# Kernel optimization log

Measured on AMD Instinct MI355X. Metric: run time of the kernel, lower is better.

Reference implementation:

```python
import jax, jax.numpy as jnp
import numpy as np
import math

B, T, C = 4, 2048, 1024
H = 16
D = C // H  # head dim = 64


def setup_inputs() -> dict:
    key = jax.random.key(0)
    k1, k2, k3 = jax.random.split(key, 3)
    x = jax.random.normal(k1, (B, T, C), dtype=jnp.float32)
    # torch nn.Linear weight layout: [out_features, in_features]
    w_attn = jax.random.normal(k2, (3 * C, C), dtype=jnp.float32) * (1.0 / math.sqrt(C))
    w_proj = jax.random.normal(k3, (C, C), dtype=jnp.float32) * (1.0 / math.sqrt(C))
    return {"x": x, "w_attn": w_attn, "w_proj": w_proj}


def reference(x, w_attn, w_proj):
    b, t, c = x.shape
    # qkv projection: Linear(C, 3C) with no bias -> x @ w_attn.T
    qkv = jnp.einsum('btc,oc->bto', x, w_attn)  # [B,T,3C]
    q, k, v = jnp.split(qkv, 3, axis=-1)
    # [B,T,C] -> [B,H,T,D]
    q = q.reshape(b, t, H, D).transpose(0, 2, 1, 3)
    k = k.reshape(b, t, H, D).transpose(0, 2, 1, 3)
    v = v.reshape(b, t, H, D).transpose(0, 2, 1, 3)
    scale = 1.0 / math.sqrt(D)
    att = jnp.einsum('bhqd,bhkd->bhqk', q, k) * scale  # [B,H,T,T]
    # NOTE: faithful to source — the naive branch applies NO causal mask
    att = jax.nn.softmax(att, axis=-1)
    y = jnp.einsum('bhqk,bhkd->bhqd', att, v)  # [B,H,T,D]
    y = y.transpose(0, 2, 1, 3).reshape(b, t, c)
    return jnp.einsum('btc,oc->bto', y, w_proj)
```

## Files before the change

### kernel.cpp

```cpp
#include <hip/hip_runtime.h>

#define T_SEQ 2048
#define C_DIM 1024
#define H_NUM 16
#define H_D   64
#define B_NUM 4
#define M_ROWS 8192

typedef __attribute__((ext_vector_type(4))) float f32x4;
typedef __attribute__((ext_vector_type(8))) short bf16x8;

__device__ __forceinline__ unsigned short f2bf(float f) {
  union { float f; unsigned int u; } a;
  a.f = f;
  unsigned int u = a.u;
  u += 0x7fffu + ((u >> 16) & 1u);
  return (unsigned short)(u >> 16);
}

__device__ __forceinline__ unsigned int fbits(float f) {
  union { float f; unsigned int u; } a; a.f = f; return a.u;
}

__device__ __forceinline__ unsigned int pack_hi(float a, float b) {
#if __has_builtin(__builtin_amdgcn_perm)
  return __builtin_amdgcn_perm(fbits(b), fbits(a), 0x07060302u);
#else
  return (fbits(b) & 0xffff0000u) | (fbits(a) >> 16);
#endif
}

__device__ __forceinline__ void gload_lds16(const unsigned short* g, unsigned short* l) {
  __builtin_amdgcn_global_load_lds(
      (const __attribute__((address_space(1))) unsigned int*)g,
      (__attribute__((address_space(3))) unsigned int*)l, 16, 0, 0);
}

__global__ __launch_bounds__(256) void cast_all_kernel(const float* __restrict__ x,
                                                       const float* __restrict__ wa,
                                                       const float* __restrict__ wp,
                                                       unsigned short* __restrict__ xb,
                                                       unsigned short* __restrict__ wab,
                                                       unsigned short* __restrict__ wpb) {
  int i = blockIdx.x * 256 + threadIdx.x;
  const float* src;
  unsigned short* dst;
  int off;
  if (i < 2097152) {
    src = x; dst = xb; off = i;
  } else if (i < 2883584) {
    src = wa; dst = wab; off = i - 2097152;
  } else {
    src = wp; dst = wpb; off = i - 2883584;
  }
  float4 v = reinterpret_cast<const float4*>(src)[off];
  ushort4 o;
  o.x = f2bf(v.x); o.y = f2bf(v.y); o.z = f2bf(v.z); o.w = f2bf(v.w);
  reinterpret_cast<ushort4*>(dst)[off] = o;
}

template <int EPI>
__global__ __launch_bounds__(256, 4) void gemm_bt_kernel(
    const unsigned short* __restrict__ A,
    const unsigned short* __restrict__ Bw,
    unsigned short* __restrict__ q_ws,
    unsigned short* __restrict__ k_ws,
    unsigned short* __restrict__ v_ws,
    float* __restrict__ outf) {
  constexpr int NN = (EPI == 0) ? 3072 : 1024;
  constexpr int KK = 1024;
  constexpr int NBC = NN / 128;
  constexpr int KT = KK / 64;

  __shared__ unsigned short lds[16384];

  const int bid = blockIdx.x;
  const int rb = bid / NBC, cb = bid % NBC;
  const int t = threadIdx.x;
  const int w = t >> 6, l = t & 63;
  const int wr = w >> 1, wc = w & 1;
  const int lq = l & 15, lg = l >> 4;

  const size_t a_base = (size_t)(rb * 128) * KK;
  const size_t b_base = (size_t)(cb * 128) * KK;

  int s_row[4], s_gs[4];
#pragma unroll
  for (int i = 0; i < 4; ++i) {
    int c = t + 256 * i;
    s_row[i] = c >> 3;
    s_gs[i] = (c & 7) ^ (s_row[i] & 7);
  }

  f32x4 acc[4][4] = {};

  for (int kt = 0; kt < KT; ++kt) {
    const int ko = kt * 64;
#pragma unroll
    for (int i = 0; i < 4; ++i) {
      unsigned short* la = &lds[(t + 256 * i) * 8];
      gload_lds16(A + a_base + (size_t)s_row[i] * KK + ko + s_gs[i] * 8, la);
      gload_lds16(Bw + b_base + (size_t)s_row[i] * KK + ko + s_gs[i] * 8, la + 8192);
    }
    __syncthreads();

#pragma unroll
    for (int kk = 0; kk < 2; ++kk) {
      const int sg = kk * 4 + lg;
      bf16x8 af[4], bfv[4];
#pragma unroll
      for (int i = 0; i < 4; ++i) {
        int R = wr * 64 + i * 16 + lq;
        af[i] = *reinterpret_cast<const bf16x8*>(&lds[(R * 8 + (sg ^ (R & 7))) * 8]);
      }
#pragma unroll
      for (int j = 0; j < 4; ++j) {
        int R = wc * 64 + j * 16 + lq;
        bfv[j] = *reinterpret_cast<const bf16x8*>(&lds[8192 + (R * 8 + (sg ^ (R & 7))) * 8]);
      }
#pragma unroll
      for (int i = 0; i < 4; ++i)
#pragma unroll
        for (int j = 0; j < 4; ++j)
          acc[i][j] = __builtin_amdgcn_mfma_f32_16x16x32_bf16(af[i], bfv[j], acc[i][j], 0, 0, 0);
    }
    __syncthreads();
  }

#pragma unroll
  for (int i = 0; i < 4; ++i) {
#pragma unroll
    for (int j = 0; j < 4; ++j) {
#pragma unroll
      for (int r = 0; r < 4; ++r) {
        int m = rb * 128 + wr * 64 + i * 16 + lg * 4 + r;
        int n = cb * 128 + wc * 64 + j * 16 + lq;
        float v = acc[i][j][r];
        if (EPI == 0) {
          int which = n >> 10;
          int h = (n >> 6) & 15;
          int d = n & 63;
          int b = m >> 11;
          int tt = m & 2047;
          int bh = b * H_NUM + h;
          if (which == 0) {
            q_ws[((size_t)bh * T_SEQ + tt) * H_D + d] = f2bf(v * 0.18033688f);
          } else if (which == 1) {
            k_ws[((size_t)bh * T_SEQ + tt) * H_D + d] = f2bf(v);
          } else {
            int k0 = tt & 63;
            int tp = (tt & ~63) | ((k0 & 12) << 1) | ((k0 & 48) >> 3) | (k0 & 1) | ((k0 & 2) << 4);
            v_ws[((size_t)bh * H_D + d) * T_SEQ + tp] = f2bf(v);
          }
        } else {
          outf[(size_t)m * 1024 + n] = v;
        }
      }
    }
  }
}

__global__ __launch_bounds__(256, 2) void attn_kernel(
    const unsigned short* __restrict__ qw,
    const unsigned short* __restrict__ kw,
    const unsigned short* __restrict__ vtw,
    unsigned short* __restrict__ yw) {
  __shared__ unsigned short kv_lds[3][8192];

  const int bid = blockIdx.x;
  const int bh = (bid & 7) * 8 + ((bid >> 3) & 7);
  const int qblk = bid >> 6;

  const int t = threadIdx.x;
  const int w = t >> 6, l = t & 63;
  const int lq = l & 15, lg = l >> 4;
  const int qbase = qblk * 256 + w * 64;
  const size_t head_off = (size_t)bh * T_SEQ * H_D;

  bf16x8 aq[4][2];
#pragma unroll
  for (int qg = 0; qg < 4; ++qg)
#pragma unroll
    for (int kk = 0; kk < 2; ++kk)
      aq[qg][kk] = *reinterpret_cast<const bf16x8*>(
          qw + head_off + (size_t)(qbase + qg * 16 + lq) * H_D + kk * 32 + lg * 8);

  const unsigned short* sbase[4];
  int sstep[4];
#pragma unroll
  for (int i = 0; i < 4; ++i) {
    int c = w * 64 + l + 256 * i;
    if (c < 512) {
      int row = c >> 3, sl = (c & 7) ^ (row & 7);
      sbase[i] = kw + head_off + row * H_D + sl * 8;
      sstep[i] = 64 * H_D;
    } else {
      int c2 = c - 512;
      int row = c2 >> 3, sl = (c2 & 7) ^ (row & 7);
      sbase[i] = vtw + head_off + (size_t)row * T_SEQ + sl * 8;
      sstep[i] = 64;
    }
  }

  unsigned short* bA = &kv_lds[0][0];
  unsigned short* bB = &kv_lds[1][0];
  unsigned short* bC = &kv_lds[2][0];

#define STAGE(KV, DST)                                                              \
  { _Pragma("unroll")                                                               \
    for (int i = 0; i < 4; ++i)                                                     \
      gload_lds16(sbase[i] + (size_t)(KV) * sstep[i], (DST) + (w * 64 + 256 * i) * 8); }

  STAGE(0, bA)
  STAGE(1, bB)

  f32x4 y[4][4] = {};
  float lrow[4] = {0.f, 0.f, 0.f, 0.f};
  union pa_t { bf16x8 v; unsigned int u[4]; };

  for (int kv = 0; kv < T_SEQ / 64; ++kv) {
    if (kv == T_SEQ / 64 - 1) {
      asm volatile("s_waitcnt vmcnt(0)" ::: "memory");
    } else {
      asm volatile("s_waitcnt vmcnt(4)" ::: "memory");
    }
    __builtin_amdgcn_s_barrier();

    bf16x8 kf[8], vf[8];
#pragma unroll
    for (int f = 0; f < 8; ++f) {
      int row = (f >> 1) * 16 + lq;
      int sl = ((f & 1) * 4 + lg) ^ (lq & 7);
      kf[f] = *reinterpret_cast<const bf16x8*>(bA + row * 64 + sl * 8);
    }
#pragma unroll
    for (int db = 0; db < 4; ++db)
#pragma unroll
      for (int ks = 0; ks < 2; ++ks) {
        int row = db * 16 + lq;
        int sl = (ks * 4 + lg) ^ (lq & 7);
        vf[db * 2 + ks] = *reinterpret_cast<const bf16x8*>(bA + 4096 + row * 64 + sl * 8);
      }

    pa_t pa0[4], pa1[4];
#pragma unroll
    for (int qg = 0; qg < 4; ++qg) {
      f32x4 s[4];
#pragma unroll
      for (int tt = 0; tt < 4; ++tt) {
        f32x4 z = {0.f, 0.f, 0.f, 0.f};
        s[tt] = __builtin_amdgcn_mfma_f32_16x16x32_bf16(kf[tt * 2], aq[qg][0], z, 0, 0, 0);
        s[tt] = __builtin_amdgcn_mfma_f32_16x16x32_bf16(kf[tt * 2 + 1], aq[qg][1], s[tt], 0, 0, 0);
      }
      float acc_e = 0.f;
#pragma unroll
      for (int tt = 0; tt < 4; ++tt) {
        float e0 = __builtin_amdgcn_exp2f(s[tt][0]);
        float e1 = __builtin_amdgcn_exp2f(s[tt][1]);
        float e2 = __builtin_amdgcn_exp2f(s[tt][2]);
        float e3 = __builtin_amdgcn_exp2f(s[tt][3]);
        pa0[qg].u[tt] = pack_hi(e0, e1);
        pa1[qg].u[tt] = pack_hi(e2, e3);
        acc_e += (e0 + e1) + (e2 + e3);
      }
      lrow[qg] += acc_e;
    }

#pragma unroll
    for (int qg = 0; qg < 4; ++qg)
#pragma unroll
      for (int db = 0; db < 4; ++db) {
        y[qg][db] = __builtin_amdgcn_mfma_f32_16x16x32_bf16(pa0[qg].v, vf[db * 2], y[qg][db], 0, 0, 0);
        y[qg][db] = __builtin_amdgcn_mfma_f32_16x16x32_bf16(pa1[qg].v, vf[db * 2 + 1], y[qg][db], 0, 0, 0);
      }

    if (kv + 2 < T_SEQ / 64) STAGE(kv + 2, bC)

    unsigned short* tmp = bA; bA = bB; bB = bC; bC = tmp;
  }
#undef STAGE

  const int b = bh >> 4, h = bh & 15;
#pragma unroll
  for (int qg = 0; qg < 4; ++qg) {
    float sm = lrow[qg];
    sm += __shfl_xor(sm, 16);
    sm += __shfl_xor(sm, 32);
    float inv = 1.0f / sm;
#pragma unroll
    for (int r = 0; r < 4; ++r) {
      float iv = __shfl(inv, lg * 4 + r);
      int row = qbase + qg * 16 + lg * 4 + r;
#pragma unroll
      for (int db = 0; db < 4; ++db) {
        int d = db * 16 + lq;
        yw[((size_t)(b * T_SEQ + row)) * C_DIM + h * 64 + d] = f2bf(y[qg][db][r] * iv);
      }
    }
  }
}

extern "C" void kernel_launch(void* const* d_in, const int* in_sizes, int n_in,
                              void* d_out, int out_size, void* d_ws, size_t ws_size,
                              hipStream_t stream) {
  (void)in_sizes; (void)n_in; (void)out_size; (void)ws_size;
  const float* x      = (const float*)d_in[0];
  const float* w_attn = (const float*)d_in[1];
  const float* w_proj = (const float*)d_in[2];
  float* out = (float*)d_out;

  unsigned short* ws = (unsigned short*)d_ws;
  const size_t XB = (size_t)M_ROWS * C_DIM;
  unsigned short* xb  = ws;
  unsigned short* wab = xb + XB;
  unsigned short* wpb = wab + (size_t)3072 * 1024;
  unsigned short* qws = wpb + (size_t)1024 * 1024;
  unsigned short* kws = qws + XB;
  unsigned short* vws = kws + XB;
  unsigned short* yws = xb;

  cast_all_kernel<<<3145728 / 256, 256, 0, stream>>>(x, w_attn, w_proj, xb, wab, wpb);

  gemm_bt_kernel<0><<<64 * 24, 256, 0, stream>>>(xb, wab, qws, kws, vws, nullptr);
  attn_kernel<<<512, 256, 0, stream>>>(qws, kws, vws, yws);
  gemm_bt_kernel<1><<<64 * 8, 256, 0, stream>>>(yws, wpb, nullptr, nullptr, nullptr, out);
}
```

Before: 178.1 us.

## Triple-buffer GEMM LDS tiles with BK=32 and async prefetch two stages ahead

The projection GEMM kernel now uses three LDS buffers holding 32-wide K slices instead of a single 64-wide buffer. Global-to-LDS loads are issued two iterations ahead, with explicit vmcnt waits and a single barrier per iteration, so loads overlap MFMA work. The LDS layout and swizzle are reworked to pack two rows per 64-element line, and launch bounds drop to 3 waves per SIMD. The cost is more barriers per unit of K, a subtle reliance on vmcnt counting and on LDS reads finishing before the buffer is overwritten, and possibly lower occupancy.

Result: slower. 186.9 us (+4.9%).

```diff
diff --git a/kernel.cpp b/kernel.cpp
--- a/kernel.cpp
+++ b/kernel.cpp
@@ -60,7 +60,7 @@
 }
 
 template <int EPI>
-__global__ __launch_bounds__(256, 4) void gemm_bt_kernel(
+__global__ __launch_bounds__(256, 3) void gemm_bt_kernel(
     const unsigned short* __restrict__ A,
     const unsigned short* __restrict__ Bw,
     unsigned short* __restrict__ q_ws,
@@ -70,9 +70,9 @@
   constexpr int NN = (EPI == 0) ? 3072 : 1024;
   constexpr int KK = 1024;
   constexpr int NBC = NN / 128;
-  constexpr int KT = KK / 64;
-
-  __shared__ unsigned short lds[16384];
+  constexpr int KT = KK / 32;
+
+  __shared__ __align__(16) unsigned short lds[3][8192];
 
   const int bid = blockIdx.x;
   const int rb = bid / NBC, cb = bid % NBC;
@@ -84,48 +84,78 @@
   const size_t a_base = (size_t)(rb * 128) * KK;
   const size_t b_base = (size_t)(cb * 128) * KK;
 
-  int s_row[4], s_gs[4];
+  const unsigned short* srcA[2];
+  const unsigned short* srcB[2];
+#pragma unroll
+  for (int i = 0; i < 2; ++i) {
+    int c = t + 256 * i;
+    int p = c >> 3;
+    int sp = (c & 7) ^ (p & 7);
+    int r = (p << 1) | (sp >> 2);
+    int s = sp & 3;
+    srcA[i] = A + a_base + (size_t)r * KK + s * 8;
+    srcB[i] = Bw + b_base + (size_t)r * KK + s * 8;
+  }
+
+  int offA[4], offB[4];
 #pragma unroll
   for (int i = 0; i < 4; ++i) {
-    int c = t + 256 * i;
-    s_row[i] = c >> 3;
-    s_gs[i] = (c & 7) ^ (s_row[i] & 7);
-  }
+    int R = wr * 64 + i * 16 + lq;
+    int p = R >> 1;
+    int sl = (((R & 1) << 2) | lg) ^ (p & 7);
+    offA[i] = p * 64 + sl * 8;
+  }
+#pragma unroll
+  for (int j = 0; j < 4; ++j) {
+    int R = wc * 64 + j * 16 + lq;
+    int p = R >> 1;
+    int sl = (((R & 1) << 2) | lg) ^ (p & 7);
+    offB[j] = 4096 + p * 64 + sl * 8;
+  }
+
+  unsigned short* bA = &lds[0][0];
+  unsigned short* bB = &lds[1][0];
+  unsigned short* bC = &lds[2][0];
+
+#define GSTAGE(KT_, DST)                                                    \
+  { _Pragma("unroll")                                                       \
+    for (int i = 0; i < 2; ++i) {                                           \
+      gload_lds16(srcA[i] + (KT_) * 32, (DST) + (t + 256 * i) * 8);         \
+      gload_lds16(srcB[i] + (KT_) * 32, (DST) + 4096 + (t + 256 * i) * 8);  \
+    } }
+
+  GSTAGE(0, bA)
+  GSTAGE(1, bB)
 
   f32x4 acc[4][4] = {};
 
   for (int kt = 0; kt < KT; ++kt) {
-    const int ko = kt * 64;
-#pragma unroll
-    for (int i = 0; i < 4; ++i) {
-      unsigned short* la = &lds[(t + 256 * i) * 8];
-      gload_lds16(A + a_base + (size_t)s_row[i] * KK + ko + s_gs[i] * 8, la);
-      gload_lds16(Bw + b_base + (size_t)s_row[i] * KK + ko + s_gs[i] * 8, la + 8192);
-    }
-    __syncthreads();
-
-#pragma unroll
-    for (int kk = 0; kk < 2; ++kk) {
-      const int sg = kk * 4 + lg;
-      bf16x8 af[4], bfv[4];
-#pragma unroll
-      for (int i = 0; i < 4; ++i) {
-        int R = wr * 64 + i * 16 + lq;
-        af[i] = *reinterpret_cast<const bf16x8*>(&lds[(R * 8 + (sg ^ (R & 7))) * 8]);
-      }
-#pragma unroll
-      for (int j = 0; j < 4; ++j) {
-        int R = wc * 64 + j * 16 + lq;
-        bfv[j] = *reinterpret_cast<const bf16x8*>(&lds[8192 + (R * 8 + (sg ^ (R & 7))) * 8]);
-      }
-#pragma unroll
-      for (int i = 0; i < 4; ++i)
-#pragma unroll
-        for (int j = 0; j < 4; ++j)
-          acc[i][j] = __builtin_amdgcn_mfma_f32_16x16x32_bf16(af[i], bfv[j], acc[i][j], 0, 0, 0);
-    }
-    __syncthreads();
-  }
+    if (kt == KT - 1) {
+      asm volatile("s_waitcnt vmcnt(0)" ::: "memory");
+    } else {
+      asm volatile("s_waitcnt vmcnt(4)" ::: "memory");
+    }
+    __builtin_amdgcn_s_barrier();
+
+    bf16x8 af[4], bfv[4];
+#pragma unroll
+    for (int i = 0; i < 4; ++i)
+      af[i] = *reinterpret_cast<const bf16x8*>(bA + offA[i]);
+#pragma unroll
+    for (int j = 0; j < 4; ++j)
+      bfv[j] = *reinterpret_cast<const bf16x8*>(bA + offB[j]);
+
+#pragma unroll
+    for (int i = 0; i < 4; ++i)
+#pragma unroll
+      for (int j = 0; j < 4; ++j)
+        acc[i][j] = __builtin_amdgcn_mfma_f32_16x16x32_bf16(af[i], bfv[j], acc[i][j], 0, 0, 0);
+
+    if (kt + 2 < KT) GSTAGE(kt + 2, bC)
+
+    unsigned short* tmp = bA; bA = bB; bB = bC; bC = tmp;
+  }
+#undef GSTAGE
 
 #pragma unroll
   for (int i = 0; i < 4; ++i) {
```

## Rewrite projection GEMMs as 8-wave double-buffered pipelined kernels with larger tiles

Applied to the files above, without the earlier changes.

Replaces the 128x128 single-buffered GEMM with a 512-thread kernel using 256xBN tiles (BN=192 for QKV, 128 for output). It double-buffers the LDS and issues global-to-LDS loads for the next k-tile between MFMA phases, using explicit vmcnt waits, barriers and setprio. Block indices are remapped so groups of neighbouring blocks share operands in cache. The aim is to hide load latency and improve data reuse. The cost is more LDS per block, lower occupancy, and fragile hand-placed wait counts.

Measured after the change: 188.5 us. +5.9%, slower.

```diff
diff --git a/kernel.cpp b/kernel.cpp
--- a/kernel.cpp
+++ b/kernel.cpp
@@ -35,6 +35,10 @@
       (const __attribute__((address_space(1))) unsigned int*)g,
       (__attribute__((address_space(3))) unsigned int*)l, 16, 0, 0);
 }
+
+#define VMC(n) asm volatile("s_waitcnt vmcnt(" #n ")" ::: "memory")
+#define LG0()  asm volatile("s_waitcnt lgkmcnt(0)" ::: "memory")
+#define BAR()  __builtin_amdgcn_s_barrier()
 
 __global__ __launch_bounds__(256) void cast_all_kernel(const float* __restrict__ x,
                                                        const float* __restrict__ wa,
@@ -60,82 +64,166 @@
 }
 
 template <int EPI>
-__global__ __launch_bounds__(256, 4) void gemm_bt_kernel(
+__global__ __launch_bounds__(512, 2) void gemm8p_kernel(
     const unsigned short* __restrict__ A,
     const unsigned short* __restrict__ Bw,
     unsigned short* __restrict__ q_ws,
     unsigned short* __restrict__ k_ws,
     unsigned short* __restrict__ v_ws,
     float* __restrict__ outf) {
-  constexpr int NN = (EPI == 0) ? 3072 : 1024;
-  constexpr int KK = 1024;
-  constexpr int NBC = NN / 128;
-  constexpr int KT = KK / 64;
-
-  __shared__ unsigned short lds[16384];
+  constexpr int BN  = (EPI == 0) ? 192 : 128;
+  constexpr int NF  = BN / 64;
+  constexpr int BLD = (BN * 64 * 2) / (512 * 16);
+  constexpr int KK  = 1024;
+  constexpr int KT  = KK / 64;
+  constexpr int NBC = (EPI == 0) ? 16 : 8;
+  constexpr int NWG = 32 * NBC;
+  constexpr int LDSZ = 16384 + BN * 64;
+
+  __shared__ __align__(16) unsigned short lds[2][LDSZ];
 
   const int bid = blockIdx.x;
-  const int rb = bid / NBC, cb = bid % NBC;
+  const int logical = (bid & 7) * (NWG / 8) + (bid >> 3);
+  const int rb = logical / NBC, cb = logical % NBC;
+
   const int t = threadIdx.x;
   const int w = t >> 6, l = t & 63;
-  const int wr = w >> 1, wc = w & 1;
+  const int wr = w >> 2, wc = w & 3;
   const int lq = l & 15, lg = l >> 4;
 
-  const size_t a_base = (size_t)(rb * 128) * KK;
-  const size_t b_base = (size_t)(cb * 128) * KK;
-
-  int s_row[4], s_gs[4];
-#pragma unroll
-  for (int i = 0; i < 4; ++i) {
-    int c = t + 256 * i;
-    s_row[i] = c >> 3;
-    s_gs[i] = (c & 7) ^ (s_row[i] & 7);
-  }
-
-  f32x4 acc[4][4] = {};
+  const size_t a_base = (size_t)(rb * 256) * KK;
+  const size_t b_base = (size_t)(cb * BN) * KK;
+
+  const unsigned short* srcA[2][2];
+#pragma unroll
+  for (int h = 0; h < 2; ++h)
+#pragma unroll
+    for (int i = 0; i < 2; ++i) {
+      int c = t + 512 * i;
+      int row = c >> 3;
+      int sw = (c & 7) ^ (row & 7);
+      srcA[h][i] = A + a_base + (size_t)(h * 128 + row) * KK + sw * 8;
+    }
+  const unsigned short* srcB[BLD];
+#pragma unroll
+  for (int i = 0; i < BLD; ++i) {
+    int c = t + 512 * i;
+    int row = c >> 3;
+    int sw = (c & 7) ^ (row & 7);
+    srcB[i] = Bw + b_base + (size_t)row * KK + sw * 8;
+  }
+
+#define STAGE_AH(DSTBUF, H, KTILE)                                            \
+  { _Pragma("unroll")                                                         \
+    for (int i_ = 0; i_ < 2; ++i_)                                            \
+      gload_lds16(srcA[H][i_] + (KTILE) * 64,                                 \
+                  (DSTBUF) + (H) * 8192 + (t + 512 * i_) * 8); }
+
+#define STAGE_B(DSTBUF, KTILE)                                                \
+  { _Pragma("unroll")                                                         \
+    for (int i_ = 0; i_ < BLD; ++i_)                                          \
+      gload_lds16(srcB[i_] + (KTILE) * 64,                                    \
+                  (DSTBUF) + 16384 + (t + 512 * i_) * 8); }
+
+  const int sw0 = ((0 * 4 + lg) ^ (lq & 7)) * 8;
+  const int sw1 = ((1 * 4 + lg) ^ (lq & 7)) * 8;
+  const int arow = (wr * 128 + lq) * 64;
+  const int brow = 16384 + (wc * (BN / 4) + lq) * 64;
+
+#define LOAD_AF(MQ, SW)                                                       \
+  { _Pragma("unroll")                                                         \
+    for (int i_ = 0; i_ < 4; ++i_)                                            \
+      af[i_] = *reinterpret_cast<const bf16x8*>(                              \
+          cur + arow + ((MQ) * 4096 + i_ * 1024) + (SW)); }
+
+#define LOAD_BF(SW)                                                           \
+  { _Pragma("unroll")                                                         \
+    for (int j_ = 0; j_ < NF; ++j_)                                           \
+      bfv[j_] = *reinterpret_cast<const bf16x8*>(cur + brow + j_ * 1024 + (SW)); }
+
+#define MM(MQ)                                                                \
+  { _Pragma("unroll")                                                         \
+    for (int i_ = 0; i_ < 4; ++i_)                                            \
+      _Pragma("unroll")                                                       \
+      for (int j_ = 0; j_ < NF; ++j_)                                         \
+        acc[(MQ) * 4 + i_][j_] = __builtin_amdgcn_mfma_f32_16x16x32_bf16(     \
+            af[i_], bfv[j_], acc[(MQ) * 4 + i_][j_], 0, 0, 0); }
+
+  STAGE_B(&lds[0][0], 0)
+  STAGE_AH(&lds[0][0], 0, 0)
+  STAGE_AH(&lds[0][0], 1, 0)
+  STAGE_B(&lds[1][0], 1)
+  if constexpr (BLD == 3) { VMC(3); } else { VMC(2); }
+  BAR();
+
+  f32x4 acc[8][NF] = {};
 
   for (int kt = 0; kt < KT; ++kt) {
-    const int ko = kt * 64;
-#pragma unroll
-    for (int i = 0; i < 4; ++i) {
-      unsigned short* la = &lds[(t + 256 * i) * 8];
-      gload_lds16(A + a_base + (size_t)s_row[i] * KK + ko + s_gs[i] * 8, la);
-      gload_lds16(Bw + b_base + (size_t)s_row[i] * KK + ko + s_gs[i] * 8, la + 8192);
-    }
-    __syncthreads();
-
-#pragma unroll
-    for (int kk = 0; kk < 2; ++kk) {
-      const int sg = kk * 4 + lg;
-      bf16x8 af[4], bfv[4];
-#pragma unroll
-      for (int i = 0; i < 4; ++i) {
-        int R = wr * 64 + i * 16 + lq;
-        af[i] = *reinterpret_cast<const bf16x8*>(&lds[(R * 8 + (sg ^ (R & 7))) * 8]);
-      }
-#pragma unroll
-      for (int j = 0; j < 4; ++j) {
-        int R = wc * 64 + j * 16 + lq;
-        bfv[j] = *reinterpret_cast<const bf16x8*>(&lds[8192 + (R * 8 + (sg ^ (R & 7))) * 8]);
-      }
-#pragma unroll
-      for (int i = 0; i < 4; ++i)
-#pragma unroll
-        for (int j = 0; j < 4; ++j)
-          acc[i][j] = __builtin_amdgcn_mfma_f32_16x16x32_bf16(af[i], bfv[j], acc[i][j], 0, 0, 0);
-    }
-    __syncthreads();
-  }
-
-#pragma unroll
-  for (int i = 0; i < 4; ++i) {
-#pragma unroll
-    for (int j = 0; j < 4; ++j) {
+    unsigned short* cur = &lds[kt & 1][0];
+    unsigned short* oth = &lds[(kt & 1) ^ 1][0];
+    bf16x8 bfv[NF];
+    {
+      bf16x8 af[4];
+      LOAD_AF(0, sw0)
+      LOAD_BF(sw0)
+      if (kt + 1 < KT) STAGE_AH(oth, 0, kt + 1)
+      BAR(); LG0();
+      __builtin_amdgcn_s_setprio(1);
+      MM(0)
+      __builtin_amdgcn_s_setprio(0);
+      BAR();
+    }
+    {
+      bf16x8 af[4];
+      LOAD_AF(1, sw0)
+      if (kt + 1 < KT) STAGE_AH(oth, 1, kt + 1)
+      BAR(); LG0();
+      __builtin_amdgcn_s_setprio(1);
+      MM(1)
+      __builtin_amdgcn_s_setprio(0);
+      BAR();
+    }
+    {
+      bf16x8 af[4];
+      LOAD_AF(0, sw1)
+      LOAD_BF(sw1)
+      BAR(); LG0();
+      __builtin_amdgcn_s_setprio(1);
+      MM(0)
+      __builtin_amdgcn_s_setprio(0);
+      BAR();
+    }
+    {
+      bf16x8 af[4];
+      LOAD_AF(1, sw1)
+      if (kt + 2 < KT) STAGE_B(cur, kt + 2)
+      BAR(); LG0();
+      __builtin_amdgcn_s_setprio(1);
+      MM(1)
+      __builtin_amdgcn_s_setprio(0);
+      if (kt < KT - 2) {
+        if constexpr (BLD == 3) { VMC(3); } else { VMC(2); }
+      } else if (kt == KT - 2) {
+        VMC(0);
+      }
+      BAR();
+    }
+  }
+#undef STAGE_AH
+#undef STAGE_B
+#undef LOAD_AF
+#undef LOAD_BF
+#undef MM
+
+#pragma unroll
+  for (int f = 0; f < 8; ++f) {
+#pragma unroll
+    for (int j = 0; j < NF; ++j) {
 #pragma unroll
       for (int r = 0; r < 4; ++r) {
-        int m = rb * 128 + wr * 64 + i * 16 + lg * 4 + r;
-        int n = cb * 128 + wc * 64 + j * 16 + lq;
-        float v = acc[i][j][r];
+        int m = rb * 256 + wr * 128 + f * 16 + lg * 4 + r;
+        int n = cb * BN + wc * (BN / 4) + j * 16 + lq;
+        float v = acc[f][j][r];
         if (EPI == 0) {
           int which = n >> 10;
           int h = (n >> 6) & 15;
@@ -321,7 +409,7 @@
 
   cast_all_kernel<<<3145728 / 256, 256, 0, stream>>>(x, w_attn, w_proj, xb, wab, wpb);
 
-  gemm_bt_kernel<0><<<64 * 24, 256, 0, stream>>>(xb, wab, qws, kws, vws, nullptr);
+  gemm8p_kernel<0><<<512, 512, 0, stream>>>(xb, wab, qws, kws, vws, nullptr);
   attn_kernel<<<512, 256, 0, stream>>>(qws, kws, vws, yws);
-  gemm_bt_kernel<1><<<64 * 8, 256, 0, stream>>>(yws, wpb, nullptr, nullptr, nullptr, out);
-}
+  gemm8p_kernel<1><<<256, 512, 0, stream>>>(yws, wpb, nullptr, nullptr, nullptr, out);
+}
```

## Split QKV GEMM into larger 256x192 tile kernel with XCD-aware block remap

Applied to the files above, without the earlier changes.

Replaces the templated GEMM with a dedicated QKV kernel that uses 512 threads and 256x192 output tiles (512 blocks instead of 1536), raising operand reuse per LDS load. Both GEMMs also remap block IDs so consecutive blocks on the same XCD share row/column panels, improving L2 locality. The larger tile uses more LDS (56KB) and more accumulator registers per thread, which may reduce occupancy and limit latency hiding.

After: 190.8 us. 7.1% more time.

```diff
diff --git a/kernel.cpp b/kernel.cpp
--- a/kernel.cpp
+++ b/kernel.cpp
@@ -59,23 +59,128 @@
   reinterpret_cast<ushort4*>(dst)[off] = o;
 }
 
-template <int EPI>
-__global__ __launch_bounds__(256, 4) void gemm_bt_kernel(
+__global__ __launch_bounds__(512, 4) void gemm_qkv_kernel(
     const unsigned short* __restrict__ A,
     const unsigned short* __restrict__ Bw,
     unsigned short* __restrict__ q_ws,
     unsigned short* __restrict__ k_ws,
-    unsigned short* __restrict__ v_ws,
+    unsigned short* __restrict__ v_ws) {
+  constexpr int KK = 1024;
+  constexpr int KT = KK / 64;
+
+  __shared__ unsigned short lds[16384 + 12288];
+
+  const int bid = blockIdx.x;
+  const int logical = (bid & 7) * 64 + (bid >> 3);
+  const int rb = logical >> 4, cb = logical & 15;
+
+  const int t = threadIdx.x;
+  const int w = t >> 6, l = t & 63;
+  const int wr = w >> 2, wc = w & 3;
+  const int lq = l & 15, lg = l >> 4;
+
+  const size_t a_base = (size_t)(rb * 256) * KK;
+  const size_t b_base = (size_t)(cb * 192) * KK;
+
+  int aRow[4], aGs[4];
+#pragma unroll
+  for (int i = 0; i < 4; ++i) {
+    int c = t + 512 * i;
+    aRow[i] = c >> 3;
+    aGs[i] = (c & 7) ^ (aRow[i] & 7);
+  }
+  int bRow[3], bGs[3];
+#pragma unroll
+  for (int i = 0; i < 3; ++i) {
+    int c = t + 512 * i;
+    bRow[i] = c >> 3;
+    bGs[i] = (c & 7) ^ (bRow[i] & 7);
+  }
+
+  f32x4 acc[8][3] = {};
+
+  for (int kt = 0; kt < KT; ++kt) {
+    const int ko = kt * 64;
+#pragma unroll
+    for (int i = 0; i < 4; ++i)
+      gload_lds16(A + a_base + (size_t)aRow[i] * KK + ko + aGs[i] * 8,
+                  &lds[(t + 512 * i) * 8]);
+#pragma unroll
+    for (int i = 0; i < 3; ++i)
+      gload_lds16(Bw + b_base + (size_t)bRow[i] * KK + ko + bGs[i] * 8,
+                  &lds[16384 + (t + 512 * i) * 8]);
+    __syncthreads();
+
+#pragma unroll
+    for (int kk = 0; kk < 2; ++kk) {
+      const int sg = kk * 4 + lg;
+      bf16x8 bfv[3];
+#pragma unroll
+      for (int j = 0; j < 3; ++j) {
+        int R = wc * 48 + j * 16 + lq;
+        bfv[j] = *reinterpret_cast<const bf16x8*>(&lds[16384 + (R * 8 + (sg ^ (R & 7))) * 8]);
+      }
+#pragma unroll
+      for (int mq = 0; mq < 2; ++mq) {
+        bf16x8 af[4];
+#pragma unroll
+        for (int i = 0; i < 4; ++i) {
+          int R = wr * 128 + mq * 64 + i * 16 + lq;
+          af[i] = *reinterpret_cast<const bf16x8*>(&lds[(R * 8 + (sg ^ (R & 7))) * 8]);
+        }
+#pragma unroll
+        for (int i = 0; i < 4; ++i)
+#pragma unroll
+          for (int j = 0; j < 3; ++j)
+            acc[mq * 4 + i][j] =
+                __builtin_amdgcn_mfma_f32_16x16x32_bf16(af[i], bfv[j], acc[mq * 4 + i][j], 0, 0, 0);
+      }
+    }
+    __syncthreads();
+  }
+
+#pragma unroll
+  for (int f = 0; f < 8; ++f) {
+#pragma unroll
+    for (int j = 0; j < 3; ++j) {
+#pragma unroll
+      for (int r = 0; r < 4; ++r) {
+        int m = rb * 256 + wr * 128 + f * 16 + lg * 4 + r;
+        int n = cb * 192 + wc * 48 + j * 16 + lq;
+        float v = acc[f][j][r];
+        int which = n >> 10;
+        int h = (n >> 6) & 15;
+        int d = n & 63;
+        int b = m >> 11;
+        int tt = m & 2047;
+        int bh = b * H_NUM + h;
+        if (which == 0) {
+          q_ws[((size_t)bh * T_SEQ + tt) * H_D + d] = f2bf(v * 0.18033688f);
+        } else if (which == 1) {
+          k_ws[((size_t)bh * T_SEQ + tt) * H_D + d] = f2bf(v);
+        } else {
+          int k0 = tt & 63;
+          int tp = (tt & ~63) | ((k0 & 12) << 1) | ((k0 & 48) >> 3) | (k0 & 1) | ((k0 & 2) << 4);
+          v_ws[((size_t)bh * H_D + d) * T_SEQ + tp] = f2bf(v);
+        }
+      }
+    }
+  }
+}
+
+__global__ __launch_bounds__(256, 4) void gemm_proj_kernel(
+    const unsigned short* __restrict__ A,
+    const unsigned short* __restrict__ Bw,
     float* __restrict__ outf) {
-  constexpr int NN = (EPI == 0) ? 3072 : 1024;
   constexpr int KK = 1024;
-  constexpr int NBC = NN / 128;
   constexpr int KT = KK / 64;
 
   __shared__ unsigned short lds[16384];
 
   const int bid = blockIdx.x;
-  const int rb = bid / NBC, cb = bid % NBC;
+  const int logical = (bid & 7) * 64 + (bid >> 3);
+  const int rb = logical >> 3, cb = logical & 7;
+
   const int t = threadIdx.x;
   const int w = t >> 6, l = t & 63;
   const int wr = w >> 1, wc = w & 1;
@@ -128,36 +233,15 @@
   }
 
 #pragma unroll
-  for (int i = 0; i < 4; ++i) {
-#pragma unroll
-    for (int j = 0; j < 4; ++j) {
+  for (int i = 0; i < 4; ++i)
+#pragma unroll
+    for (int j = 0; j < 4; ++j)
 #pragma unroll
       for (int r = 0; r < 4; ++r) {
         int m = rb * 128 + wr * 64 + i * 16 + lg * 4 + r;
         int n = cb * 128 + wc * 64 + j * 16 + lq;
-        float v = acc[i][j][r];
-        if (EPI == 0) {
-          int which = n >> 10;
-          int h = (n >> 6) & 15;
-          int d = n & 63;
-          int b = m >> 11;
-          int tt = m & 2047;
-          int bh = b * H_NUM + h;
-          if (which == 0) {
-            q_ws[((size_t)bh * T_SEQ + tt) * H_D + d] = f2bf(v * 0.18033688f);
-          } else if (which == 1) {
-            k_ws[((size_t)bh * T_SEQ + tt) * H_D + d] = f2bf(v);
-          } else {
-            int k0 = tt & 63;
-            int tp = (tt & ~63) | ((k0 & 12) << 1) | ((k0 & 48) >> 3) | (k0 & 1) | ((k0 & 2) << 4);
-            v_ws[((size_t)bh * H_D + d) * T_SEQ + tp] = f2bf(v);
-          }
-        } else {
-          outf[(size_t)m * 1024 + n] = v;
-        }
-      }
-    }
-  }
+        outf[(size_t)m * 1024 + n] = acc[i][j][r];
+      }
 }
 
 __global__ __launch_bounds__(256, 2) void attn_kernel(
@@ -321,7 +405,7 @@
 
   cast_all_kernel<<<3145728 / 256, 256, 0, stream>>>(x, w_attn, w_proj, xb, wab, wpb);
 
-  gemm_bt_kernel<0><<<64 * 24, 256, 0, stream>>>(xb, wab, qws, kws, vws, nullptr);
+  gemm_qkv_kernel<<<512, 512, 0, stream>>>(xb, wab, qws, kws, vws);
   attn_kernel<<<512, 256, 0, stream>>>(qws, kws, vws, yws);
-  gemm_bt_kernel<1><<<64 * 8, 256, 0, stream>>>(yws, wpb, nullptr, nullptr, nullptr, out);
-}
+  gemm_proj_kernel<<<512, 256, 0, stream>>>(yws, wpb, out);
+}
```
